# Performance work log

Hardware: AMD Instinct MI355X
Metric: run time of the kernel (lower is better)

## Reference

```python
import jax, jax.numpy as jnp
import numpy as np

N_HEAD = 16
NUM_GROUPS = 2


def setup_inputs() -> dict:
    key = jax.random.key(0)
    k1, k2, k3 = jax.random.split(key, 3)
    B, T, D = 4, 2048, 1024
    x = jax.random.normal(k1, (B, T, D), dtype=jnp.float32)
    W_attn = jax.random.normal(k2, (D, 3 * D), dtype=jnp.float32) * 0.02
    b_attn = jnp.zeros((3 * D,), dtype=jnp.float32)
    W_proj = jax.random.normal(k3, (D, D), dtype=jnp.float32) * 0.02
    b_proj = jnp.zeros((D,), dtype=jnp.float32)
    return {"x": x, "W_attn": W_attn, "b_attn": b_attn, "W_proj": W_proj, "b_proj": b_proj}


def _rope_tables(T, d_head):
    # thetas = 1000 ** (-2*arange(1, d/2+1)/d), repeat_interleave(2); positions start at 1
    half = d_head // 2
    thetas = 1000.0 ** (-2.0 * jnp.arange(1, half + 1, dtype=jnp.float32) / d_head)
    thetas = jnp.repeat(thetas, 2)                      # (d_head,)
    pos = jnp.arange(1, T + 1, dtype=jnp.float32)       # (T,)
    args = pos[:, None] * thetas[None, :]               # (T, d_head)
    return jnp.sin(args), jnp.cos(args)


def _apply_rope(x, sin, cos):
    # x: (B, H, T, d_head)
    x_odd = x[..., ::2]
    x_even = x[..., 1::2]
    x_sin = jnp.stack([-x_even, x_odd], axis=-1).reshape(x.shape)  # [-x1, x0, -x3, x2, ...]
    return x * cos + x_sin * sin


def reference(x, W_attn, b_attn, W_proj, b_proj):
    B, T, D = x.shape
    H = N_HEAD
    hd = D // H
    group_dim = D // NUM_GROUPS  # scale divisor; split degenerates to one group since group_dim >= hd

    qkv = x @ W_attn + b_attn                              # (B, T, 3D)
    q, k, v = jnp.split(qkv, 3, axis=-1)

    def split_heads(t):
        return t.reshape(B, T, H, hd).transpose(0, 2, 1, 3)  # (B, H, T, hd)

    q, k, v = split_heads(q), split_heads(k), split_heads(v)

    sin, cos = _rope_tables(T, hd)
    q = _apply_rope(q, sin, cos)
    k = _apply_rope(k, sin, cos)

    # NOTE: original forward never applies the causal mask (attn_mask=None) -> full softmax
    scores = jnp.einsum('bhqd,bhkd->bhqk', q, k) / jnp.sqrt(jnp.float32(group_dim))
    attn = jax.nn.softmax(scores, axis=-1)
    out = jnp.einsum('bhqk,bhkd->bhqd', attn, v)           # (B, H, T, hd)

    out = out.transpose(0, 2, 1, 3).reshape(B, T, D)       # merge heads
    return out @ W_proj + b_proj
```

## Files before the change

kernel.cpp:

```cpp
#include <hip/hip_runtime.h>
#include <hip/hip_bf16.h>
#include <stdint.h>

#define DEVI __device__ __forceinline__

using bf16x8 = __attribute__((ext_vector_type(8))) short;
using f32x4  = __attribute__((ext_vector_type(4))) float;
using f16x4  = __attribute__((ext_vector_type(4))) _Float16;
using f16x8  = __attribute__((ext_vector_type(8))) _Float16;

static constexpr int Bc = 4;
static constexpr int Tc = 2048;
static constexpr int Dc = 1024;
static constexpr int Hc = 16;
static constexpr int HDc = 64;
#define QSCALE 0.06375788883274286f

#if __has_builtin(__builtin_amdgcn_exp2f)
#define EXP2F __builtin_amdgcn_exp2f
#else
#define EXP2F exp2f
#endif

typedef const unsigned int __attribute__((address_space(1)))* gas1_t;
typedef unsigned int __attribute__((address_space(3)))* las3_t;

DEVI void gld16(const void* g, void* l)
{
    __builtin_amdgcn_global_load_lds((gas1_t)(uintptr_t)g, (las3_t)(uintptr_t)l, 16, 0, 0);
}


__global__ void f2bf_kernel(const float4* __restrict__ x, ushort4* __restrict__ y, int n4)
{
    const int base = blockIdx.x * 1024 + threadIdx.x;
#pragma unroll
    for (int u = 0; u < 4; u++) {
        const int i = base + u * 256;
        float4 v = x[i];
        union { __hip_bfloat16 h[4]; ushort4 u4; } cv;
        cv.h[0] = __float2bfloat16(v.x);
        cv.h[1] = __float2bfloat16(v.y);
        cv.h[2] = __float2bfloat16(v.z);
        cv.h[3] = __float2bfloat16(v.w);
        y[i] = cv.u4;
    }
}

__global__ void transpose_bf_kernel(const float* __restrict__ W, __hip_bfloat16* __restrict__ Wt,
                                    int K, int N)
{
    __shared__ float tile[64][65];
    const int n0 = blockIdx.x * 64, k0 = blockIdx.y * 64;
    const int tx = threadIdx.x & 15, ty = threadIdx.x >> 4;
#pragma unroll
    for (int i2 = 0; i2 < 4; i2++) {
        const int k = ty + 16 * i2;
        float4 v = *(const float4*)&W[(size_t)(k0 + k) * N + n0 + tx * 4];
        tile[tx * 4 + 0][k] = v.x;
        tile[tx * 4 + 1][k] = v.y;
        tile[tx * 4 + 2][k] = v.z;
        tile[tx * 4 + 3][k] = v.w;
    }
    __syncthreads();
#pragma unroll
    for (int i2 = 0; i2 < 4; i2++) {
        const int n = ty + 16 * i2;
        union { __hip_bfloat16 h[4]; ushort4 u4; } cv;
#pragma unroll
        for (int c = 0; c < 4; c++)
            cv.h[c] = (__hip_bfloat16)tile[n][tx * 4 + c];
        *(ushort4*)&Wt[(size_t)(n0 + n) * K + k0 + tx * 4] = cv.u4;
    }
}

__global__ void rope_tab_kernel(float* __restrict__ sinT, float* __restrict__ cosT)
{
    int i = blockIdx.x * blockDim.x + threadIdx.x;
    int t = i >> 6, dim = i & 63;
    int p = dim >> 1;
    float theta = powf(1000.f, -2.f * (float)(p + 1) / 64.f);
    float arg = (float)(t + 1) * theta;
    sinT[i] = sinf(arg);
    cosT[i] = cosf(arg);
}


template <int MODE>
__global__ __launch_bounds__(256, 2) void gemm128(
    const __hip_bfloat16* __restrict__ A, const __hip_bfloat16* __restrict__ Bt,
    const float* __restrict__ bias, int M, int N, int K,
    const float* __restrict__ sinT, const float* __restrict__ cosT,
    __hip_bfloat16* __restrict__ Qb, __hip_bfloat16* __restrict__ Kb,
    _Float16* __restrict__ Vb, float* __restrict__ Cout)
{
    __shared__ __align__(16) __hip_bfloat16 sA[128 * 64];
    __shared__ __align__(16) __hip_bfloat16 sB[128 * 64];
    const int tid = threadIdx.x;
    const int wave = tid >> 6, lane = tid & 63;
    const int qd = lane >> 4, lm = lane & 15;
    const int wm = (wave >> 1) * 64, wn = (wave & 1) * 64;
    const int tileM = blockIdx.y * 128, tileN = blockIdx.x * 128;

    const int srow = tid >> 3;
    const int scol = (tid & 7) * 8;

    f32x4 acc[4][4];
#pragma unroll
    for (int i = 0; i < 4; i++)
#pragma unroll
        for (int j = 0; j < 4; j++)
            acc[i][j] = (f32x4){0.f, 0.f, 0.f, 0.f};

    const __hip_bfloat16* pa = A + (size_t)(tileM + srow) * K + scol;
    const __hip_bfloat16* pb = Bt + (size_t)(tileN + srow) * K + scol;

    for (int k0 = 0; k0 < K; k0 += 64) {
#pragma unroll
        for (int it = 0; it < 4; it++) {
            gld16(pa + (size_t)(it * 32) * K + k0, &sA[it * 2048 + wave * 512]);
            gld16(pb + (size_t)(it * 32) * K + k0, &sB[it * 2048 + wave * 512]);
        }
        __syncthreads();
#pragma unroll
        for (int ks = 0; ks < 2; ks++) {
            bf16x8 wf[4], xf[4];
#pragma unroll
            for (int a = 0; a < 4; a++)
                wf[a] = *(const bf16x8*)&sB[(wn + a * 16 + lm) * 64 + ks * 32 + qd * 8];
#pragma unroll
            for (int b = 0; b < 4; b++)
                xf[b] = *(const bf16x8*)&sA[(wm + b * 16 + lm) * 64 + ks * 32 + qd * 8];
#pragma unroll
            for (int a = 0; a < 4; a++)
#pragma unroll
                for (int b = 0; b < 4; b++)
                    acc[a][b] = __builtin_amdgcn_mfma_f32_16x16x32_bf16(
                        wf[a], xf[b], acc[a][b], 0, 0, 0);
        }
        __syncthreads();
    }

    if constexpr (MODE == 0) {
        const int sec = tileN >> 10;
        const int h = ((tileN + wn) & 1023) >> 6;
#pragma unroll
        for (int a = 0; a < 4; a++) {
            const int dim0 = a * 16 + qd * 4;
            const int n0 = tileN + wn + dim0;
            const float4 bi = *(const float4*)&bias[n0];
#pragma unroll
            for (int b = 0; b < 4; b++) {
                const int m = tileM + wm + b * 16 + lm;
                const int t = m & (Tc - 1), bb = m >> 11;
                const float v0 = acc[a][b][0] + bi.x;
                const float v1 = acc[a][b][1] + bi.y;
                const float v2 = acc[a][b][2] + bi.z;
                const float v3 = acc[a][b][3] + bi.w;
                if (sec < 2) {
                    const float4 sn = *(const float4*)&sinT[t * 64 + dim0];
                    const float4 cs = *(const float4*)&cosT[t * 64 + dim0];
                    const float o0 = v0 * cs.x - v1 * sn.x;
                    const float o1 = v1 * cs.y + v0 * sn.y;
                    const float o2 = v2 * cs.z - v3 * sn.z;
                    const float o3 = v3 * cs.w + v2 * sn.w;
                    union { __hip_bfloat16 hx[4]; ushort4 u4; } cv;
                    if (sec == 0) {
                        cv.hx[0] = (__hip_bfloat16)(o0 * QSCALE);
                        cv.hx[1] = (__hip_bfloat16)(o1 * QSCALE);
                        cv.hx[2] = (__hip_bfloat16)(o2 * QSCALE);
                        cv.hx[3] = (__hip_bfloat16)(o3 * QSCALE);
                        *(ushort4*)&Qb[((size_t)(bb * Hc + h) * Tc + t) * HDc + dim0] = cv.u4;
                    } else {
                        cv.hx[0] = (__hip_bfloat16)o0;
                        cv.hx[1] = (__hip_bfloat16)o1;
                        cv.hx[2] = (__hip_bfloat16)o2;
                        cv.hx[3] = (__hip_bfloat16)o3;
                        const int dswb = dim0 ^ ((t & 7) << 3);
                        *(ushort4*)&Kb[((size_t)(bb * Hc + h) * Tc + t) * HDc + dswb] = cv.u4;
                    }
                } else {
                    const int u = t & 31;
                    const int posA = (t & ~31) + (((u & 15) >> 2) << 3)
                                     + ((u >> 4) << 2) + (u & 3);
                    const float vv[4] = {v0, v1, v2, v3};
#pragma unroll
                    for (int r = 0; r < 4; r++) {
                        const int dim = dim0 + r;
                        const int pos = posA ^ ((dim & 7) << 3);
                        Vb[((size_t)(bb * Hc + h) * HDc + dim) * Tc + pos] = (_Float16)vv[r];
                    }
                }
            }
        }
    } else {
#pragma unroll
        for (int a = 0; a < 4; a++) {
            const int n0 = tileN + wn + a * 16 + qd * 4;
            const float4 bi = *(const float4*)&bias[n0];
#pragma unroll
            for (int b = 0; b < 4; b++) {
                const int m = tileM + wm + b * 16 + lm;
                float4 o;
                o.x = acc[a][b][0] + bi.x;
                o.y = acc[a][b][1] + bi.y;
                o.z = acc[a][b][2] + bi.z;
                o.w = acc[a][b][3] + bi.w;
                *(float4*)&Cout[(size_t)m * N + n0] = o;
            }
        }
    }
}


__global__ __launch_bounds__(256, 2) void attn_kernel(
    const __hip_bfloat16* __restrict__ Qb, const __hip_bfloat16* __restrict__ Kb,
    const _Float16* __restrict__ Vh, __hip_bfloat16* __restrict__ AO)
{
    __shared__ __align__(16) __hip_bfloat16 sK[2][64 * 64];
    __shared__ __align__(16) _Float16 sV[2][64 * 64];
    const int tid = threadIdx.x, wave = tid >> 6, lane = tid & 63;
    const int qd = lane >> 4, lm = lane & 15;
    const int i = blockIdx.x;
    const int c = i & 7, j = i >> 3;
    const int bh = c + 8 * (j >> 3);
    const int qblk = j & 7;
    const int q0 = qblk * 256 + wave * 64;

    const __hip_bfloat16* Qp = Qb + (size_t)bh * Tc * HDc;
    const __hip_bfloat16* Kp = Kb + (size_t)bh * Tc * HDc;
    const _Float16* Vp = Vh + (size_t)bh * HDc * Tc;

    bf16x8 qf[4][2];
#pragma unroll
    for (int qn = 0; qn < 4; qn++)
#pragma unroll
        for (int ks = 0; ks < 2; ks++)
            qf[qn][ks] = *(const bf16x8*)(Qp + (size_t)(q0 + qn * 16 + lm) * HDc
                                          + ks * 32 + qd * 8);

    f32x4 o[4][4];
    f32x4 lsum[4];
#pragma unroll
    for (int qn = 0; qn < 4; qn++) {
#pragma unroll
        for (int cb = 0; cb < 4; cb++) o[qn][cb] = (f32x4){0.f, 0.f, 0.f, 0.f};
        lsum[qn] = (f32x4){0.f, 0.f, 0.f, 0.f};
    }
    const f16x8 one8 = {(_Float16)1.f, (_Float16)1.f, (_Float16)1.f, (_Float16)1.f,
                        (_Float16)1.f, (_Float16)1.f, (_Float16)1.f, (_Float16)1.f};

    const int swl = (lm & 7) << 3;

    auto stage = [&](int p, int k0) {
        const char* gK = (const char*)(Kp + (size_t)k0 * HDc);
#pragma unroll
        for (int jj = 0; jj < 2; jj++) {
            const int call = wave * 2 + jj;
            gld16(gK + call * 1024 + lane * 16,
                  (char*)&sK[p][0] + call * 1024 + lane * 16);
            const int dim = call * 8 + (lane >> 3);
            gld16((const char*)(Vp + (size_t)dim * Tc + k0 + (lane & 7) * 8),
                  (char*)&sV[p][0] + call * 1024 + lane * 16);
        }
    };

    stage(0, 0);

    for (int kt = 0; kt < Tc / 64; kt++) {
        const int p = kt & 1;
        if (kt < Tc / 64 - 1) {
            stage(p ^ 1, (kt + 1) * 64);
            __builtin_amdgcn_s_waitcnt(0xF74);
        } else {
            __builtin_amdgcn_s_waitcnt(0xF70);
        }
        __builtin_amdgcn_s_barrier();

        const __hip_bfloat16* bK = &sK[p][0];
        const _Float16* bV = &sV[p][0];

        f16x8 pf8[4][2];
#pragma unroll
        for (int g = 0; g < 2; g++) {
#pragma unroll
            for (int hh = 0; hh < 2; hh++) {
                const int krow = (2 * g + hh) * 16 + lm;
                bf16x8 kf0 = *(const bf16x8*)&bK[krow * 64 + ((0 + qd * 8) ^ swl)];
                bf16x8 kf1 = *(const bf16x8*)&bK[krow * 64 + ((32 + qd * 8) ^ swl)];
#pragma unroll
                for (int qn = 0; qn < 4; qn++) {
                    f32x4 s = (f32x4){0.f, 0.f, 0.f, 0.f};
                    s = __builtin_amdgcn_mfma_f32_16x16x32_bf16(kf0, qf[qn][0], s, 0, 0, 0);
                    s = __builtin_amdgcn_mfma_f32_16x16x32_bf16(kf1, qf[qn][1], s, 0, 0, 0);
                    auto lo = __builtin_amdgcn_cvt_pkrtz(EXP2F(s[0]), EXP2F(s[1]));
                    auto hi = __builtin_amdgcn_cvt_pkrtz(EXP2F(s[2]), EXP2F(s[3]));
                    pf8[qn][g][4 * hh + 0] = lo[0];
                    pf8[qn][g][4 * hh + 1] = lo[1];
                    pf8[qn][g][4 * hh + 2] = hi[0];
                    pf8[qn][g][4 * hh + 3] = hi[1];
                }
            }
        }

#pragma unroll
        for (int qn = 0; qn < 4; qn++)
#pragma unroll
            for (int g = 0; g < 2; g++)
                lsum[qn] = __builtin_amdgcn_mfma_f32_16x16x32_f16(
                    one8, pf8[qn][g], lsum[qn], 0, 0, 0);

#pragma unroll
        for (int g = 0; g < 2; g++) {
#pragma unroll
            for (int cb = 0; cb < 4; cb++) {
                f16x8 v8 = *(const f16x8*)&bV[(cb * 16 + lm) * 64
                                              + ((g * 32 + qd * 8) ^ swl)];
#pragma unroll
                for (int qn = 0; qn < 4; qn++)
                    o[qn][cb] = __builtin_amdgcn_mfma_f32_16x16x32_f16(
                        v8, pf8[qn][g], o[qn][cb], 0, 0, 0);
            }
        }
        __builtin_amdgcn_s_barrier();
    }

    const int b = bh >> 4, h = bh & 15;
#pragma unroll
    for (int qn = 0; qn < 4; qn++) {
        const float rinv = 1.f / lsum[qn][0];
        const int t = q0 + qn * 16 + lm;
#pragma unroll
        for (int cb = 0; cb < 4; cb++)
#pragma unroll
            for (int r = 0; r < 4; r++) {
                const int dim = cb * 16 + qd * 4 + r;
                AO[((size_t)b * Tc + t) * Dc + h * HDc + dim] =
                    (__hip_bfloat16)(o[qn][cb][r] * rinv);
            }
    }
}


extern "C" void kernel_launch(void* const* d_in, const int* in_sizes, int n_in,
                              void* d_out, int out_size, void* d_ws, size_t ws_size,
                              hipStream_t stream)
{
    const float* x      = (const float*)d_in[0];
    const float* W_attn = (const float*)d_in[1];
    const float* b_attn = (const float*)d_in[2];
    const float* W_proj = (const float*)d_in[3];
    const float* b_proj = (const float*)d_in[4];
    float* out = (float*)d_out;

    char* w = (char*)d_ws;
    auto alloc = [&](size_t bytes) -> char* {
        char* p = w;
        w += (bytes + 255) & ~(size_t)255;
        return p;
    };
    __hip_bfloat16* xb  = (__hip_bfloat16*)alloc((size_t)Bc * Tc * Dc * 2);
    __hip_bfloat16* Wqt = (__hip_bfloat16*)alloc((size_t)3 * Dc * Dc * 2);
    __hip_bfloat16* Wpt = (__hip_bfloat16*)alloc((size_t)Dc * Dc * 2);
    __hip_bfloat16* Qb  = (__hip_bfloat16*)alloc((size_t)Bc * Hc * Tc * HDc * 2);
    __hip_bfloat16* Kb  = (__hip_bfloat16*)alloc((size_t)Bc * Hc * Tc * HDc * 2);
    _Float16*       Vh  = (_Float16*)alloc((size_t)Bc * Hc * Tc * HDc * 2);
    __hip_bfloat16* AO  = (__hip_bfloat16*)alloc((size_t)Bc * Tc * Dc * 2);
    float* sinT = (float*)alloc((size_t)Tc * 64 * 4);
    float* cosT = (float*)alloc((size_t)Tc * 64 * 4);

    const int M = Bc * Tc;

    f2bf_kernel<<<dim3((M * Dc / 4) / 1024), dim3(256), 0, stream>>>(
        (const float4*)x, (ushort4*)xb, M * Dc / 4);
    transpose_bf_kernel<<<dim3(3 * Dc / 64, Dc / 64), dim3(256), 0, stream>>>(
        W_attn, Wqt, Dc, 3 * Dc);
    transpose_bf_kernel<<<dim3(Dc / 64, Dc / 64), dim3(256), 0, stream>>>(
        W_proj, Wpt, Dc, Dc);
    rope_tab_kernel<<<dim3(Tc * 64 / 256), dim3(256), 0, stream>>>(sinT, cosT);

    gemm128<0><<<dim3(3 * Dc / 128, M / 128), dim3(256), 0, stream>>>(
        xb, Wqt, b_attn, M, 3 * Dc, Dc, sinT, cosT, Qb, Kb, Vh, nullptr);

    attn_kernel<<<dim3(512), dim3(256), 0, stream>>>(Qb, Kb, Vh, AO);

    gemm128<1><<<dim3(Dc / 128, M / 128), dim3(256), 0, stream>>>(
        AO, Wpt, b_proj, M, Dc, Dc, nullptr, nullptr, nullptr, nullptr, nullptr, out);
}
```

Measured before the change: 267.1 us.

## Double-buffer GEMM LDS tiles and XOR-swizzle to avoid bank conflicts

```diff
diff --git a/kernel.cpp b/kernel.cpp
--- a/kernel.cpp
+++ b/kernel.cpp
@@ -94,8 +94,8 @@
     __hip_bfloat16* __restrict__ Qb, __hip_bfloat16* __restrict__ Kb,
     _Float16* __restrict__ Vb, float* __restrict__ Cout)
 {
-    __shared__ __align__(16) __hip_bfloat16 sA[128 * 64];
-    __shared__ __align__(16) __hip_bfloat16 sB[128 * 64];
+    __shared__ __align__(16) __hip_bfloat16 sA[2][128 * 64];
+    __shared__ __align__(16) __hip_bfloat16 sB[2][128 * 64];
     const int tid = threadIdx.x;
     const int wave = tid >> 6, lane = tid & 63;
     const int qd = lane >> 4, lm = lane & 15;
@@ -103,7 +103,7 @@
     const int tileM = blockIdx.y * 128, tileN = blockIdx.x * 128;
 
     const int srow = tid >> 3;
-    const int scol = (tid & 7) * 8;
+    const int socc = (tid & 7) ^ (srow & 7);
 
     f32x4 acc[4][4];
 #pragma unroll
@@ -112,25 +112,42 @@
         for (int j = 0; j < 4; j++)
             acc[i][j] = (f32x4){0.f, 0.f, 0.f, 0.f};
 
-    const __hip_bfloat16* pa = A + (size_t)(tileM + srow) * K + scol;
-    const __hip_bfloat16* pb = Bt + (size_t)(tileN + srow) * K + scol;
-
-    for (int k0 = 0; k0 < K; k0 += 64) {
+    const __hip_bfloat16* pa = A + (size_t)(tileM + srow) * K + socc * 8;
+    const __hip_bfloat16* pb = Bt + (size_t)(tileN + srow) * K + socc * 8;
+
+    auto stageT = [&](int p, int k0) {
 #pragma unroll
         for (int it = 0; it < 4; it++) {
-            gld16(pa + (size_t)(it * 32) * K + k0, &sA[it * 2048 + wave * 512]);
-            gld16(pb + (size_t)(it * 32) * K + k0, &sB[it * 2048 + wave * 512]);
-        }
-        __syncthreads();
+            gld16(pa + (size_t)(it * 32) * K + k0, &sA[p][it * 2048 + wave * 512]);
+            gld16(pb + (size_t)(it * 32) * K + k0, &sB[p][it * 2048 + wave * 512]);
+        }
+    };
+
+    stageT(0, 0);
+
+    const int swl = (lm & 7) << 3;
+    const int nk = K / 64;
+    for (int kt = 0; kt < nk; kt++) {
+        const int p = kt & 1;
+        if (kt + 1 < nk) {
+            stageT(p ^ 1, (kt + 1) * 64);
+            __builtin_amdgcn_s_waitcnt(0xF78);
+        } else {
+            __builtin_amdgcn_s_waitcnt(0xF70);
+        }
+        __builtin_amdgcn_s_barrier();
+
 #pragma unroll
         for (int ks = 0; ks < 2; ks++) {
             bf16x8 wf[4], xf[4];
 #pragma unroll
             for (int a = 0; a < 4; a++)
-                wf[a] = *(const bf16x8*)&sB[(wn + a * 16 + lm) * 64 + ks * 32 + qd * 8];
+                wf[a] = *(const bf16x8*)&sB[p][(wn + a * 16 + lm) * 64
+                                              + ((ks * 32 + qd * 8) ^ swl)];
 #pragma unroll
             for (int b = 0; b < 4; b++)
-                xf[b] = *(const bf16x8*)&sA[(wm + b * 16 + lm) * 64 + ks * 32 + qd * 8];
+                xf[b] = *(const bf16x8*)&sA[p][(wm + b * 16 + lm) * 64
+                                              + ((ks * 32 + qd * 8) ^ swl)];
 #pragma unroll
             for (int a = 0; a < 4; a++)
 #pragma unroll
@@ -138,7 +155,7 @@
                     acc[a][b] = __builtin_amdgcn_mfma_f32_16x16x32_bf16(
                         wf[a], xf[b], acc[a][b], 0, 0, 0);
         }
-        __syncthreads();
+        __builtin_amdgcn_s_barrier();
     }
 
     if constexpr (MODE == 0) {
```

New measurement: 267.8 us. Within noise of the previous version (+0.2%).
